# Kernel tuning notes

Hardware: AMD Instinct MI355X
Metric: run time of the kernel (lower is better)

The kernel has to match this reference:

```python
import jax, jax.numpy as jnp
import numpy as np

B, S, D = 4, 2048, 1024

def setup_inputs() -> dict:
    key = jax.random.key(0)
    ks = jax.random.split(key, 7)
    scale = 1.0 / np.sqrt(D)
    return {
        "x": jax.random.normal(ks[0], (B, S, D), dtype=jnp.float32),
        "Wq": jax.random.uniform(ks[1], (D, D), jnp.float32, -scale, scale),
        "bq": jax.random.uniform(ks[2], (D,), jnp.float32, -scale, scale),
        "Wk": jax.random.uniform(ks[3], (D, D), jnp.float32, -scale, scale),
        "bk": jax.random.uniform(ks[4], (D,), jnp.float32, -scale, scale),
        "Wv": jax.random.uniform(ks[5], (D, D), jnp.float32, -scale, scale),
        "bv": jax.random.uniform(ks[6], (D,), jnp.float32, -scale, scale),
    }

def reference(x, Wq, bq, Wk, bk, Wv, bv):
    # Linear layers: x @ W^T + b (torch nn.Linear convention)
    q = jnp.einsum('bsd,ed->bse', x, Wq) + bq  # [B,S,D]
    k = jnp.einsum('bsd,ed->bse', x, Wk) + bk
    v = jnp.einsum('bsd,ed->bse', x, Wv) + bv
    inv_sqrt_d = 1.0 / jnp.sqrt(jnp.asarray(k.shape[-1], k.dtype))
    scores = jnp.einsum('bqd,bkd->bqk', q, k) * inv_sqrt_d  # [B,S,S]
    attn = jax.nn.softmax(scores, axis=-1)
    return jnp.einsum('bqk,bkd->bqd', attn, v)
```

## Files before the change

kernel.cpp:

```cpp
#include <hip/hip_runtime.h>
#include <cstdint>


typedef __bf16 bf16x8_t __attribute__((ext_vector_type(8)));
typedef float  f32x4_t  __attribute__((ext_vector_type(4)));

__device__ __forceinline__ uint16_t f2bf(float f) {
    union { float f; uint32_t u; } v; v.f = f;
    return (uint16_t)((v.u + 0x7fffu + ((v.u >> 16) & 1u)) >> 16);
}
__device__ __forceinline__ float bf2f(uint16_t u) {
    union { uint32_t u; float f; } v; v.u = ((uint32_t)u) << 16;
    return v.f;
}

__device__ __forceinline__ void gload_lds16(const uint16_t* g, uint16_t* lds) {
    __builtin_amdgcn_global_load_lds(
        (const __attribute__((address_space(1))) void*)g,
        (__attribute__((address_space(3))) void*)lds, 16, 0, 0);
}

template <int BIAS, typename OutT>
__global__ __launch_bounds__(256, 3) void gemm_bt(
    const uint16_t* __restrict__ A, int lda, long long sAz,
    const uint16_t* __restrict__ B, int ldb, long long sBz,
    OutT* __restrict__ C, int ldc, long long sCz,
    const float* __restrict__ bias0, const float* __restrict__ bias1,
    int K, float alpha)
{
    __shared__ uint16_t ldsA[128 * 32];
    __shared__ uint16_t ldsB[128 * 32];

    const int tid  = threadIdx.x;
    const int wave = tid >> 6;
    const int lane = tid & 63;
    const int quad = lane >> 4;
    const int l15  = lane & 15;
    const int z    = blockIdx.z;

    A += (long long)z * sAz;
    B += (long long)z * sBz;
    C += (long long)z * sCz;

    const int m0 = blockIdx.x * 128;
    const int n0 = blockIdx.y * 128;

    const int sA0 = (0 * 4 + wave) * 64 + lane;
    const int sA1 = (1 * 4 + wave) * 64 + lane;
    const int r0 = sA0 >> 2, c0 = (sA0 & 3) * 8;
    const int r1 = sA1 >> 2, c1 = (sA1 & 3) * 8;

    const uint16_t* gA0 = A + (long long)(m0 + r0) * lda + c0;
    const uint16_t* gA1 = A + (long long)(m0 + r1) * lda + c1;
    const uint16_t* gB0 = B + (long long)(n0 + r0) * ldb + c0;
    const uint16_t* gB1 = B + (long long)(n0 + r1) * ldb + c1;

    uint16_t* lA0 = ldsA + (0 * 4 + wave) * 512;
    uint16_t* lA1 = ldsA + (1 * 4 + wave) * 512;
    uint16_t* lB0 = ldsB + (0 * 4 + wave) * 512;
    uint16_t* lB1 = ldsB + (1 * 4 + wave) * 512;

    const int m_off = (wave & 1) * 64;
    const int n_off = (wave >> 1) * 64;

    f32x4_t acc[4][4];
#pragma unroll
    for (int i = 0; i < 4; ++i)
#pragma unroll
        for (int j = 0; j < 4; ++j)
            acc[i][j] = f32x4_t{0.f, 0.f, 0.f, 0.f};

    for (int k0 = 0; k0 < K; k0 += 32) {
        gload_lds16(gA0, lA0);
        gload_lds16(gA1, lA1);
        gload_lds16(gB0, lB0);
        gload_lds16(gB1, lB1);
        gA0 += 32; gA1 += 32; gB0 += 32; gB1 += 32;
        __syncthreads();

        bf16x8_t af[4], bfr[4];
#pragma unroll
        for (int i = 0; i < 4; ++i)
            af[i] = *(const bf16x8_t*)(ldsA + (m_off + i * 16 + l15) * 32 + quad * 8);
#pragma unroll
        for (int j = 0; j < 4; ++j)
            bfr[j] = *(const bf16x8_t*)(ldsB + (n_off + j * 16 + l15) * 32 + quad * 8);
#pragma unroll
        for (int i = 0; i < 4; ++i)
#pragma unroll
            for (int j = 0; j < 4; ++j)
                acc[i][j] = __builtin_amdgcn_mfma_f32_16x16x32_bf16(af[i], bfr[j], acc[i][j], 0, 0, 0);
        __syncthreads();
    }

    const float* bias = (z == 0) ? bias0 : bias1;
#pragma unroll
    for (int i = 0; i < 4; ++i) {
        const int mb = m0 + m_off + i * 16 + quad * 4;
        float rb[4];
        if (BIAS == 2) {
#pragma unroll
            for (int r = 0; r < 4; ++r) rb[r] = bias[mb + r];
        }
#pragma unroll
        for (int j = 0; j < 4; ++j) {
            const int n = n0 + n_off + j * 16 + l15;
            float cb = 0.f;
            if (BIAS == 1) cb = bias[n];
#pragma unroll
            for (int r = 0; r < 4; ++r) {
                float v = acc[i][j][r] * alpha;
                if (BIAS == 1) v += cb;
                if (BIAS == 2) v += rb[r];
                if (sizeof(OutT) == 2)
                    ((uint16_t*)C)[(long long)(mb + r) * ldc + n] = f2bf(v);
                else
                    ((float*)C)[(long long)(mb + r) * ldc + n] = v;
            }
        }
    }
}

__global__ void cvt_x(const float* __restrict__ src, uint16_t* __restrict__ dst) {
    const int i = blockIdx.x * 256 + threadIdx.x;
    const float4 f = ((const float4*)src)[i];
    ushort4 o;
    o.x = f2bf(f.x); o.y = f2bf(f.y); o.z = f2bf(f.z); o.w = f2bf(f.w);
    ((ushort4*)dst)[i] = o;
}

__global__ void cvt_w(const float* __restrict__ Wq, const float* __restrict__ Wk,
                      const float* __restrict__ Wv, uint16_t* __restrict__ dst) {
    const int z = blockIdx.z;
    const float* s = (z == 0) ? Wq : (z == 1) ? Wk : Wv;
    const int i = blockIdx.x * 256 + threadIdx.x;
    const float4 f = ((const float4*)s)[i];
    ushort4 o;
    o.x = f2bf(f.x); o.y = f2bf(f.y); o.z = f2bf(f.z); o.w = f2bf(f.w);
    ((ushort4*)(dst + (long long)z * 1048576))[i] = o;
}

__global__ __launch_bounds__(256) void softmax_rows(uint16_t* __restrict__ S) {
    uint16_t* p = S + (long long)blockIdx.x * 2048;
    const int tid  = threadIdx.x;
    const int wave = tid >> 6;
    const int lane = tid & 63;

    float v[8];
#pragma unroll
    for (int i = 0; i < 8; ++i) v[i] = bf2f(p[tid + i * 256]);

    float m = v[0];
#pragma unroll
    for (int i = 1; i < 8; ++i) m = fmaxf(m, v[i]);
#pragma unroll
    for (int off = 32; off > 0; off >>= 1) m = fmaxf(m, __shfl_xor(m, off));

    __shared__ float red[8];
    if (lane == 0) red[wave] = m;
    __syncthreads();
    m = fmaxf(fmaxf(red[0], red[1]), fmaxf(red[2], red[3]));

    float s = 0.f;
#pragma unroll
    for (int i = 0; i < 8; ++i) {
        v[i] = exp2f((v[i] - m) * 1.4426950408889634f);
        s += v[i];
    }
#pragma unroll
    for (int off = 32; off > 0; off >>= 1) s += __shfl_xor(s, off);
    if (lane == 0) red[4 + wave] = s;
    __syncthreads();
    s = red[4] + red[5] + red[6] + red[7];
    const float inv = 1.f / s;
#pragma unroll
    for (int i = 0; i < 8; ++i) p[tid + i * 256] = f2bf(v[i] * inv);
}

extern "C" void kernel_launch(void* const* d_in, const int* in_sizes, int n_in,
                              void* d_out, int out_size, void* d_ws, size_t ws_size,
                              hipStream_t stream) {
    const float* x  = (const float*)d_in[0];
    const float* Wq = (const float*)d_in[1];
    const float* bq = (const float*)d_in[2];
    const float* Wk = (const float*)d_in[3];
    const float* bk = (const float*)d_in[4];
    const float* Wv = (const float*)d_in[5];
    const float* bv = (const float*)d_in[6];
    float* out = (float*)d_out;

    char* w = (char*)d_ws;
    uint16_t* x_bf = (uint16_t*)(w);
    uint16_t* w_bf = (uint16_t*)(w + 16777216);
    uint16_t* Qb   = (uint16_t*)(w + 23068672);
    uint16_t* Kb   = (uint16_t*)(w + 39845888);
    uint16_t* Vt   = (uint16_t*)(w + 56623104);
    uint16_t* Sb   = (uint16_t*)(w + 73400320);

    cvt_x<<<8192, 256, 0, stream>>>(x, x_bf);
    cvt_w<<<dim3(1024, 1, 3), 256, 0, stream>>>(Wq, Wk, Wv, w_bf);

    gemm_bt<1, uint16_t><<<dim3(64, 8, 2), 256, 0, stream>>>(
        x_bf, 1024, 0LL,
        w_bf, 1024, 1048576LL,
        Qb, 1024, 8388608LL,
        bq, bk, 1024, 1.0f);

    gemm_bt<2, uint16_t><<<dim3(8, 64, 1), 256, 0, stream>>>(
        w_bf + 2097152, 1024, 0LL,
        x_bf, 1024, 0LL,
        Vt, 8192, 0LL,
        bv, bv, 1024, 1.0f);

    gemm_bt<0, uint16_t><<<dim3(16, 16, 4), 256, 0, stream>>>(
        Qb, 1024, 2097152LL,
        Kb, 1024, 2097152LL,
        Sb, 2048, 4194304LL,
        nullptr, nullptr, 1024, 0.03125f);

    softmax_rows<<<8192, 256, 0, stream>>>(Sb);

    gemm_bt<0, float><<<dim3(16, 8, 4), 256, 0, stream>>>(
        Sb, 2048, 4194304LL,
        Vt, 8192, 2048LL,
        out, 1024, 2097152LL,
        nullptr, nullptr, 2048, 1.0f);
}
```

Measured before the change: 278.0 us.

## Double GEMM K-tile with XOR-swizzled LDS, fuse conversions, vectorize softmax

```diff
diff --git a/kernel.cpp b/kernel.cpp
--- a/kernel.cpp
+++ b/kernel.cpp
@@ -28,8 +28,8 @@
     const float* __restrict__ bias0, const float* __restrict__ bias1,
     int K, float alpha)
 {
-    __shared__ uint16_t ldsA[128 * 32];
-    __shared__ uint16_t ldsB[128 * 32];
+    __shared__ uint16_t ldsA[128 * 64];
+    __shared__ uint16_t ldsB[128 * 64];
 
     const int tid  = threadIdx.x;
     const int wave = tid >> 6;
@@ -45,20 +45,20 @@
     const int m0 = blockIdx.x * 128;
     const int n0 = blockIdx.y * 128;
 
-    const int sA0 = (0 * 4 + wave) * 64 + lane;
-    const int sA1 = (1 * 4 + wave) * 64 + lane;
-    const int r0 = sA0 >> 2, c0 = (sA0 & 3) * 8;
-    const int r1 = sA1 >> 2, c1 = (sA1 & 3) * 8;
-
-    const uint16_t* gA0 = A + (long long)(m0 + r0) * lda + c0;
-    const uint16_t* gA1 = A + (long long)(m0 + r1) * lda + c1;
-    const uint16_t* gB0 = B + (long long)(n0 + r0) * ldb + c0;
-    const uint16_t* gB1 = B + (long long)(n0 + r1) * ldb + c1;
-
-    uint16_t* lA0 = ldsA + (0 * 4 + wave) * 512;
-    uint16_t* lA1 = ldsA + (1 * 4 + wave) * 512;
-    uint16_t* lB0 = ldsB + (0 * 4 + wave) * 512;
-    uint16_t* lB1 = ldsB + (1 * 4 + wave) * 512;
+    const uint16_t* gA[4];
+    const uint16_t* gB[4];
+    uint16_t* lA[4];
+    uint16_t* lB[4];
+#pragma unroll
+    for (int c = 0; c < 4; ++c) {
+        const int s   = (c * 4 + wave) * 64 + lane;
+        const int r   = s >> 3;
+        const int col = ((s & 7) ^ (r & 7)) * 8;
+        gA[c] = A + (long long)(m0 + r) * lda + col;
+        gB[c] = B + (long long)(n0 + r) * ldb + col;
+        lA[c] = ldsA + (c * 4 + wave) * 512;
+        lB[c] = ldsB + (c * 4 + wave) * 512;
+    }
 
     const int m_off = (wave & 1) * 64;
     const int n_off = (wave >> 1) * 64;
@@ -70,26 +70,31 @@
         for (int j = 0; j < 4; ++j)
             acc[i][j] = f32x4_t{0.f, 0.f, 0.f, 0.f};
 
-    for (int k0 = 0; k0 < K; k0 += 32) {
-        gload_lds16(gA0, lA0);
-        gload_lds16(gA1, lA1);
-        gload_lds16(gB0, lB0);
-        gload_lds16(gB1, lB1);
-        gA0 += 32; gA1 += 32; gB0 += 32; gB1 += 32;
+    for (int k0 = 0; k0 < K; k0 += 64) {
+#pragma unroll
+        for (int c = 0; c < 4; ++c) gload_lds16(gA[c], lA[c]);
+#pragma unroll
+        for (int c = 0; c < 4; ++c) gload_lds16(gB[c], lB[c]);
+#pragma unroll
+        for (int c = 0; c < 4; ++c) { gA[c] += 64; gB[c] += 64; }
         __syncthreads();
 
-        bf16x8_t af[4], bfr[4];
-#pragma unroll
-        for (int i = 0; i < 4; ++i)
-            af[i] = *(const bf16x8_t*)(ldsA + (m_off + i * 16 + l15) * 32 + quad * 8);
-#pragma unroll
-        for (int j = 0; j < 4; ++j)
-            bfr[j] = *(const bf16x8_t*)(ldsB + (n_off + j * 16 + l15) * 32 + quad * 8);
-#pragma unroll
-        for (int i = 0; i < 4; ++i)
+#pragma unroll
+        for (int t = 0; t < 2; ++t) {
+            const int csw = (((t * 4 + quad) ^ (l15 & 7))) * 8;
+            bf16x8_t af[4], bfr[4];
+#pragma unroll
+            for (int i = 0; i < 4; ++i)
+                af[i] = *(const bf16x8_t*)(ldsA + (m_off + i * 16 + l15) * 64 + csw);
 #pragma unroll
             for (int j = 0; j < 4; ++j)
-                acc[i][j] = __builtin_amdgcn_mfma_f32_16x16x32_bf16(af[i], bfr[j], acc[i][j], 0, 0, 0);
+                bfr[j] = *(const bf16x8_t*)(ldsB + (n_off + j * 16 + l15) * 64 + csw);
+#pragma unroll
+            for (int i = 0; i < 4; ++i)
+#pragma unroll
+                for (int j = 0; j < 4; ++j)
+                    acc[i][j] = __builtin_amdgcn_mfma_f32_16x16x32_bf16(af[i], bfr[j], acc[i][j], 0, 0, 0);
+        }
         __syncthreads();
     }
 
@@ -121,23 +126,27 @@
     }
 }
 
-__global__ void cvt_x(const float* __restrict__ src, uint16_t* __restrict__ dst) {
-    const int i = blockIdx.x * 256 + threadIdx.x;
+__global__ void cvt_all(const float* __restrict__ x,
+                        const float* __restrict__ Wq, const float* __restrict__ Wk,
+                        const float* __restrict__ Wv,
+                        uint16_t* __restrict__ x_bf, uint16_t* __restrict__ w_bf) {
+    const int b = blockIdx.x;
+    const float* src;
+    uint16_t* dst;
+    int i;
+    if (b < 8192) {
+        src = x; dst = x_bf; i = b * 256 + threadIdx.x;
+    } else {
+        const int wz = (b - 8192) >> 10;
+        const int rb = (b - 8192) & 1023;
+        src = (wz == 0) ? Wq : (wz == 1) ? Wk : Wv;
+        dst = w_bf + (long long)wz * 1048576;
+        i = rb * 256 + threadIdx.x;
+    }
     const float4 f = ((const float4*)src)[i];
     ushort4 o;
     o.x = f2bf(f.x); o.y = f2bf(f.y); o.z = f2bf(f.z); o.w = f2bf(f.w);
     ((ushort4*)dst)[i] = o;
-}
-
-__global__ void cvt_w(const float* __restrict__ Wq, const float* __restrict__ Wk,
-                      const float* __restrict__ Wv, uint16_t* __restrict__ dst) {
-    const int z = blockIdx.z;
-    const float* s = (z == 0) ? Wq : (z == 1) ? Wk : Wv;
-    const int i = blockIdx.x * 256 + threadIdx.x;
-    const float4 f = ((const float4*)s)[i];
-    ushort4 o;
-    o.x = f2bf(f.x); o.y = f2bf(f.y); o.z = f2bf(f.z); o.w = f2bf(f.w);
-    ((ushort4*)(dst + (long long)z * 1048576))[i] = o;
 }
 
 __global__ __launch_bounds__(256) void softmax_rows(uint16_t* __restrict__ S) {
@@ -146,9 +155,10 @@
     const int wave = tid >> 6;
     const int lane = tid & 63;
 
-    float v[8];
-#pragma unroll
-    for (int i = 0; i < 8; ++i) v[i] = bf2f(p[tid + i * 256]);
+    const ushort4 a0 = *(const ushort4*)(p + tid * 8);
+    const ushort4 a1 = *(const ushort4*)(p + tid * 8 + 4);
+    float v[8] = {bf2f(a0.x), bf2f(a0.y), bf2f(a0.z), bf2f(a0.w),
+                  bf2f(a1.x), bf2f(a1.y), bf2f(a1.z), bf2f(a1.w)};
 
     float m = v[0];
 #pragma unroll
@@ -173,8 +183,14 @@
     __syncthreads();
     s = red[4] + red[5] + red[6] + red[7];
     const float inv = 1.f / s;
-#pragma unroll
-    for (int i = 0; i < 8; ++i) p[tid + i * 256] = f2bf(v[i] * inv);
+
+    ushort4 o0, o1;
+    o0.x = f2bf(v[0] * inv); o0.y = f2bf(v[1] * inv);
+    o0.z = f2bf(v[2] * inv); o0.w = f2bf(v[3] * inv);
+    o1.x = f2bf(v[4] * inv); o1.y = f2bf(v[5] * inv);
+    o1.z = f2bf(v[6] * inv); o1.w = f2bf(v[7] * inv);
+    *(ushort4*)(p + tid * 8)     = o0;
+    *(ushort4*)(p + tid * 8 + 4) = o1;
 }
 
 extern "C" void kernel_launch(void* const* d_in, const int* in_sizes, int n_in,
@@ -197,8 +213,7 @@
     uint16_t* Vt   = (uint16_t*)(w + 56623104);
     uint16_t* Sb   = (uint16_t*)(w + 73400320);
 
-    cvt_x<<<8192, 256, 0, stream>>>(x, x_bf);
-    cvt_w<<<dim3(1024, 1, 3), 256, 0, stream>>>(Wq, Wk, Wv, w_bf);
+    cvt_all<<<11264, 256, 0, stream>>>(x, Wq, Wk, Wv, x_bf, w_bf);
 
     gemm_bt<1, uint16_t><<<dim3(64, 8, 2), 256, 0, stream>>>(
         x_bf, 1024, 0LL,
```

New measurement: 239.9 us. 13.7% less time.
